# Kernel tuning notes

Measured on AMD Instinct MI355X. Metric: run time of the kernel, lower is better.

## Reference

```python
import jax, jax.numpy as jnp
import numpy as np

D_MODEL = 1024
D_STATE = 16
D_CONV = 4
EXPAND = 1
D_INNER = EXPAND * D_MODEL  # must equal D_MODEL for original dt_proj shapes to work
BATCH = 2
SEQ = 2048


def silu(x):
    return x * jax.nn.sigmoid(x)


def setup_inputs() -> dict:
    key = jax.random.key(0)
    ks = jax.random.split(key, 8)
    s = 0.02
    return {
        "x": jax.random.normal(ks[0], (BATCH, SEQ, D_MODEL), dtype=jnp.float32),
        "W_in": jax.random.normal(ks[1], (2 * D_INNER, D_MODEL), dtype=jnp.float32) * s,
        "conv_w": jax.random.normal(ks[2], (D_INNER, D_CONV), dtype=jnp.float32) * s,
        "conv_b": jnp.zeros((D_INNER,), dtype=jnp.float32),
        "W_dt": jax.random.normal(ks[3], (D_INNER, D_INNER), dtype=jnp.float32) * s,
        "b_dt": jnp.zeros((D_INNER,), dtype=jnp.float32),
        "A_log": jnp.zeros((D_INNER, D_STATE), dtype=jnp.float32),  # torch: log(ones)=0
        "Bp": jax.random.normal(ks[4], (D_INNER, D_STATE), dtype=jnp.float32),
        "Cp": jax.random.normal(ks[5], (D_INNER, D_STATE), dtype=jnp.float32),
        "Dp": jnp.ones((D_INNER,), dtype=jnp.float32),
        "W_out": jax.random.normal(ks[6], (D_MODEL, D_INNER), dtype=jnp.float32) * s,
    }


def reference(x, W_in, conv_w, conv_b, W_dt, b_dt, A_log, Bp, Cp, Dp, W_out):
    B, L, _ = x.shape
    # in_proj then split into ssm branch and gating residual
    xr = x @ W_in.T                               # (B, L, 2*D_INNER)
    x_proj, res = jnp.split(xr, 2, axis=-1)       # each (B, L, D_INNER)

    # causal depthwise conv1d (kernel D_CONV), == torch conv1d(padding=K-1)[..., :L]
    xp = jnp.pad(x_proj, ((0, 0), (D_CONV - 1, 0), (0, 0)))
    xc = conv_b + sum(conv_w[:, k] * xp[:, k:k + L, :] for k in range(D_CONV))
    xc = silu(xc)                                 # (B, L, D_INNER)

    # selective SSM scan
    delta = jax.nn.softplus(xc @ W_dt.T + b_dt)   # (B, L, D_INNER)
    A = -jnp.exp(A_log)                           # (D_INNER, D_STATE)
    dA = jnp.exp(delta[..., None] * A)            # (B, L, D_INNER, D_STATE)
    dBx = delta[..., None] * Bp * xc[..., None]   # (B, L, D_INNER, D_STATE)

    def step(h, inp):
        dA_t, dBx_t = inp                         # (B, D_INNER, D_STATE)
        h = dA_t * h + dBx_t
        y = jnp.einsum('bdn,dn->bd', h, Cp)
        return h, y

    h0 = jnp.zeros((B, D_INNER, D_STATE), dtype=x.dtype)
    _, ys = jax.lax.scan(step, h0, (dA.transpose(1, 0, 2, 3), dBx.transpose(1, 0, 2, 3)))
    x_ssm = ys.transpose(1, 0, 2) + xc * Dp       # (B, L, D_INNER)

    return (x_ssm * silu(res)) @ W_out.T          # (B, L, D_MODEL)
```

## Files before the change

kernel.cpp:

```cpp
#include <hip/hip_runtime.h>

typedef unsigned short u16;
typedef __bf16 bf16;
typedef bf16 bf16x8 __attribute__((ext_vector_type(8)));
typedef float f32x16 __attribute__((ext_vector_type(16)));

#define SEQ     2048
#define BATCH   2
#define DM      1024
#define DI      1024
#define NROW    (BATCH*SEQ)
#define NSTATE  16
#define NCHUNK  64
#define CLEN    32
#define BK      64

static_assert(SEQ == NCHUNK * CLEN, "chunking must cover SEQ");

__device__ __forceinline__ u16 f2bf(float f) {
  unsigned u = __builtin_bit_cast(unsigned, f);
  u += 0x7FFFu + ((u >> 16) & 1u);
  return (u16)(u >> 16);
}
__device__ __forceinline__ float bf2f(u16 u) {
  return __builtin_bit_cast(float, (unsigned)u << 16);
}
__device__ __forceinline__ float sigm(float x) { return 1.f / (1.f + __expf(-x)); }

__global__ __launch_bounds__(256) void k_cvt_all(
    const float* __restrict__ x, const float* __restrict__ Win,
    const float* __restrict__ Wdt, const float* __restrict__ Wout,
    u16* __restrict__ xbf, u16* __restrict__ winbf,
    u16* __restrict__ wdtbf, u16* __restrict__ woutbf)
{
  long i = (long)blockIdx.x * 256 + threadIdx.x;
  const float* src; u16* dst; long off;
  if (i < 1048576)            { src = x;    dst = xbf;    off = i; }
  else if (i < 1572864)       { src = Win;  dst = winbf;  off = i - 1048576; }
  else if (i < 1835008)       { src = Wdt;  dst = wdtbf;  off = i - 1572864; }
  else                        { src = Wout; dst = woutbf; off = i - 1835008; }
  float4 v = reinterpret_cast<const float4*>(src)[off];
  ushort4 o;
  o.x = f2bf(v.x); o.y = f2bf(v.y); o.z = f2bf(v.z); o.w = f2bf(v.w);
  reinterpret_cast<ushort4*>(dst)[off] = o;
}


__device__ __forceinline__ void gload16(const u16* g, u16* l) {
  __builtin_amdgcn_global_load_lds((const __attribute__((address_space(1))) void*)g,
                                   (__attribute__((address_space(3))) void*)l,
                                   16, 0, 0);
}

template<int EPI, int BM, int BN, int GX>
__global__ __launch_bounds__(256, 2) void k_gemm(
    const u16* __restrict__ A, const u16* __restrict__ B,
    float* __restrict__ outf, u16* __restrict__ outb, u16* __restrict__ outb2,
    const float* __restrict__ bias, int M, int N, int K)
{
  constexpr int MI_ = BM / 64;
  constexpr int NI_ = BN / 64;
  __shared__ __align__(16) u16 sA[2 * BM * BK];
  __shared__ __align__(16) u16 sB[2 * BN * BK];
  const int t = threadIdx.x;
  const int wave = t >> 6, lane = t & 63;
  const int la = lane & 31, hi = lane >> 5;
  const int wr = wave >> 1, wc = wave & 1;

  const int nwg = gridDim.x;
  const int bid = blockIdx.x;
  const int wg  = (bid & 7) * (nwg >> 3) + (bid >> 3);
  const long bm = (long)(wg / GX) * BM;
  const long bn = (long)(wg % GX) * BN;

  f32x16 acc[MI_][NI_] = {};

  const int srow = t >> 3;
  const int gslot8 = (((t & 7) ^ (srow & 7)) * 8);
  const u16* gA0 = A + (bm + srow) * (long)K + gslot8;
  const u16* gB0 = B + (bn + srow) * (long)K + gslot8;

  auto STAGE = [&](int buf, int k0) {
    #pragma unroll
    for (int i = 0; i < BM / 32; ++i)
      gload16(gA0 + (long)i * 32 * K + k0,
              &sA[buf * (BM * BK) + i * 2048 + wave * 512]);
    #pragma unroll
    for (int i = 0; i < BN / 32; ++i)
      gload16(gB0 + (long)i * 32 * K + k0,
              &sB[buf * (BN * BK) + i * 2048 + wave * 512]);
  };

  const int xr = la & 7;
  STAGE(0, 0);
  __syncthreads();
  int cur = 0;
  for (int k0 = 0; k0 < K; k0 += BK) {
    if (k0 + BK < K) STAGE(cur ^ 1, k0 + BK);
    const u16* pa = &sA[cur * (BM * BK)];
    const u16* pb = &sB[cur * (BN * BK)];
    bf16x8 af[4][MI_], bfr[4][NI_];
    #pragma unroll
    for (int ks = 0; ks < 4; ++ks) {
      const int co = ((ks * 2 + hi) ^ xr) * 8;
      #pragma unroll
      for (int mi = 0; mi < MI_; ++mi)
        af[ks][mi] = *reinterpret_cast<const bf16x8*>(
            pa + (wr * (BM / 2) + mi * 32 + la) * BK + co);
      #pragma unroll
      for (int ni = 0; ni < NI_; ++ni)
        bfr[ks][ni] = *reinterpret_cast<const bf16x8*>(
            pb + (wc * (BN / 2) + ni * 32 + la) * BK + co);
    }
    #pragma unroll
    for (int ks = 0; ks < 4; ++ks)
      #pragma unroll
      for (int mi = 0; mi < MI_; ++mi)
        #pragma unroll
        for (int ni = 0; ni < NI_; ++ni)
          acc[mi][ni] = __builtin_amdgcn_mfma_f32_32x32x16_bf16(
              af[ks][mi], bfr[ks][ni], acc[mi][ni], 0, 0, 0);
    __syncthreads();
    cur ^= 1;
  }

  #pragma unroll
  for (int mi = 0; mi < MI_; ++mi) {
    const long rowb = bm + wr * (BM / 2) + mi * 32 + 4 * hi;
    #pragma unroll
    for (int ni = 0; ni < NI_; ++ni) {
      const long col = bn + wc * (BN / 2) + ni * 32 + la;
      #pragma unroll
      for (int q = 0; q < 4; ++q)
        #pragma unroll
        for (int j = 0; j < 4; ++j) {
          const float v = acc[mi][ni][q * 4 + j];
          const long r = rowb + q * 8 + j;
          if (EPI == 0) {
            outf[r * N + col] = v;
          } else if (EPI == 1) {
            if (bn < DI) outb[r * DI + col] = f2bf(v);
            else         outb2[r * DI + (col - DI)] = f2bf(v * sigm(v));
          } else {
            float z = v + bias[col];
            outb[r * N + col] = f2bf(fmaxf(z, 0.f) + log1pf(__expf(-fabsf(z))));
          }
        }
    }
  }
}

__global__ void k_conv(const u16* __restrict__ xproj, const float* __restrict__ convw,
                       const float* __restrict__ convb, u16* __restrict__ xcbf)
{
  const int idx = blockIdx.x * 256 + threadIdx.x;
  const int d = idx & (DI - 1);
  const int m = idx >> 10;
  const int l = m & (SEQ - 1);
  float acc = convb[d];
  #pragma unroll
  for (int k = 0; k < 4; ++k) {
    int ls = l + k - 3;
    if (ls >= 0)
      acc = fmaf(convw[d * 4 + k], bf2f(xproj[(long)(m + k - 3) * DI + d]), acc);
  }
  float s = acc * sigm(acc);
  xcbf[idx] = f2bf(s);
}

__global__ __launch_bounds__(256) void k_scanA(
    const u16* __restrict__ delta, const u16* __restrict__ xc,
    const float* __restrict__ A_log, const float* __restrict__ Bp,
    float* __restrict__ hfin, float* __restrict__ sumdt_buf)
{
  const int tid = threadIdx.x, blk = blockIdx.x;
  const int d = (blk & 3) * 256 + tid;
  const int c = (blk >> 2) & (NCHUNK - 1);
  const int b = blk >> 8;
  float Aa[NSTATE], Bb[NSTATE], h[NSTATE];
  #pragma unroll
  for (int n = 0; n < NSTATE; ++n) {
    Aa[n] = -__expf(A_log[d * NSTATE + n]);
    Bb[n] = Bp[d * NSTATE + n];
    h[n] = 0.f;
  }
  const long base = ((long)(b * SEQ + c * CLEN)) * DI + d;
  float sdt = 0.f;
  for (int i = 0; i < CLEN; ++i) {
    float dt = bf2f(delta[base + (long)i * DI]);
    float x  = bf2f(xc[base + (long)i * DI]);
    sdt += dt;
    float dx = dt * x;
    #pragma unroll
    for (int n = 0; n < NSTATE; ++n) {
      float da = __expf(dt * Aa[n]);
      h[n] = fmaf(da, h[n], dx * Bb[n]);
    }
  }
  const long sb = ((long)(b * NCHUNK + c) * NSTATE) * DI + d;
  #pragma unroll
  for (int n = 0; n < NSTATE; ++n) hfin[sb + (long)n * DI] = h[n];
  sumdt_buf[(long)(b * NCHUNK + c) * DI + d] = sdt;
}

__global__ __launch_bounds__(256) void k_combine(
    const float* __restrict__ hfin, const float* __restrict__ sumdt_buf,
    const float* __restrict__ A_log, float* __restrict__ hstart)
{
  const int idx = blockIdx.x * 256 + threadIdx.x;
  const int d = idx & (DI - 1);
  const int n = (idx >> 10) & (NSTATE - 1);
  const int b = idx >> 14;
  const float Aa = -__expf(A_log[d * NSTATE + n]);
  float h = 0.f;
  for (int c = 0; c < NCHUNK; ++c) {
    const long sb = ((long)(b * NCHUNK + c) * NSTATE + n) * DI + d;
    hstart[sb] = h;
    float sdt = sumdt_buf[(long)(b * NCHUNK + c) * DI + d];
    h = fmaf(__expf(Aa * sdt), h, hfin[sb]);
  }
}

__global__ __launch_bounds__(256) void k_scanB(
    const u16* __restrict__ delta, const u16* __restrict__ xc,
    const float* __restrict__ A_log, const float* __restrict__ Bp,
    const float* __restrict__ Cp, const float* __restrict__ Dp,
    const u16* __restrict__ sres, const float* __restrict__ hstart,
    u16* __restrict__ gated)
{
  const int tid = threadIdx.x, blk = blockIdx.x;
  const int d = (blk & 3) * 256 + tid;
  const int c = (blk >> 2) & (NCHUNK - 1);
  const int b = blk >> 8;
  float Aa[NSTATE], Bb[NSTATE], Cc[NSTATE], h[NSTATE];
  #pragma unroll
  for (int n = 0; n < NSTATE; ++n) {
    Aa[n] = -__expf(A_log[d * NSTATE + n]);
    Bb[n] = Bp[d * NSTATE + n];
    Cc[n] = Cp[d * NSTATE + n];
  }
  const float Dd = Dp[d];
  const long sb = ((long)(b * NCHUNK + c) * NSTATE) * DI + d;
  #pragma unroll
  for (int n = 0; n < NSTATE; ++n) h[n] = hstart[sb + (long)n * DI];
  const long base = ((long)(b * SEQ + c * CLEN)) * DI + d;
  for (int i = 0; i < CLEN; ++i) {
    float dt = bf2f(delta[base + (long)i * DI]);
    float x  = bf2f(xc[base + (long)i * DI]);
    float dx = dt * x;
    float y = 0.f;
    #pragma unroll
    for (int n = 0; n < NSTATE; ++n) {
      float da = __expf(dt * Aa[n]);
      h[n] = fmaf(da, h[n], dx * Bb[n]);
      y = fmaf(h[n], Cc[n], y);
    }
    float xs = fmaf(x, Dd, y);
    float g = xs * bf2f(sres[base + (long)i * DI]);
    gated[base + (long)i * DI] = f2bf(g);
  }
}

extern "C" void kernel_launch(void* const* d_in, const int* in_sizes, int n_in,
                              void* d_out, int out_size, void* d_ws, size_t ws_size,
                              hipStream_t stream)
{
  const float* x      = (const float*)d_in[0];
  const float* W_in   = (const float*)d_in[1];
  const float* conv_w = (const float*)d_in[2];
  const float* conv_b = (const float*)d_in[3];
  const float* W_dt   = (const float*)d_in[4];
  const float* b_dt   = (const float*)d_in[5];
  const float* A_log  = (const float*)d_in[6];
  const float* Bp     = (const float*)d_in[7];
  const float* Cp     = (const float*)d_in[8];
  const float* Dp     = (const float*)d_in[9];
  const float* W_out  = (const float*)d_in[10];
  float* out = (float*)d_out;

  const long MD = (long)NROW * DI;

  char* ws = (char*)d_ws;
  u16*   xproj_bf = (u16*)ws;               ws += MD * 2;
  u16*   silu_bf  = (u16*)ws;               ws += MD * 2;
  u16*   delta_bf = (u16*)ws;               ws += MD * 2;
  u16*   xc_bf    = (u16*)ws;               ws += MD * 2;
  u16*   xbf      = (u16*)ws;               ws += MD * 2;
  u16*   Win_bf   = (u16*)ws;               ws += (long)2 * DI * DM * 2;
  u16*   Wdt_bf   = (u16*)ws;               ws += (long)DI * DI * 2;
  u16*   Wout_bf  = (u16*)ws;               ws += (long)DM * DI * 2;
  float* hfin     = (float*)ws;             ws += (long)BATCH * NCHUNK * NSTATE * DI * 4;
  float* sumdt    = (float*)ws;             ws += (long)BATCH * NCHUNK * DI * 4;
  float* hstart   = (float*)ws;             ws += (long)BATCH * NCHUNK * NSTATE * DI * 4;

  u16* gated = xbf;

  k_cvt_all<<<dim3(8192), dim3(256), 0, stream>>>(
      x, W_in, W_dt, W_out, xbf, Win_bf, Wdt_bf, Wout_bf);

  k_gemm<1, 128, 128, 16><<<dim3(512), dim3(256), 0, stream>>>(
      xbf, Win_bf, nullptr, xproj_bf, silu_bf, nullptr, NROW, 2 * DI, DM);

  k_conv<<<dim3((unsigned)(MD / 256)), dim3(256), 0, stream>>>(
      xproj_bf, conv_w, conv_b, xc_bf);

  k_gemm<2, 64, 64, 16><<<dim3(1024), dim3(256), 0, stream>>>(
      xc_bf, Wdt_bf, nullptr, delta_bf, nullptr, b_dt, NROW, DI, DI);

  k_scanA<<<dim3(BATCH * NCHUNK * (DI / 256)), dim3(256), 0, stream>>>(
      delta_bf, xc_bf, A_log, Bp, hfin, sumdt);
  k_combine<<<dim3(BATCH * NSTATE * DI / 256), dim3(256), 0, stream>>>(
      hfin, sumdt, A_log, hstart);
  k_scanB<<<dim3(BATCH * NCHUNK * (DI / 256)), dim3(256), 0, stream>>>(
      delta_bf, xc_bf, A_log, Bp, Cp, Dp, silu_bf, hstart, gated);

  k_gemm<0, 64, 64, 16><<<dim3(1024), dim3(256), 0, stream>>>(
      gated, Wout_bf, out, nullptr, nullptr, nullptr, NROW, DM, DI);
}
```

Baseline: 157.2 us.

## Fuse chunk-scan pass A into delta GEMM epilogue and vectorize conv

The delta GEMM epilogue now keeps the softplus outputs in shared memory and runs the first chunked-scan pass inside the same block. Each block handles two 32-step chunks over 64 channels, with two threads per channel each owning 8 states. This removes the separate k_scanA launch and its re-read of delta from global memory. The conv kernel now processes 8 channels per thread with vector loads and stores, setprio is raised around the MFMA loop, and the output GEMM gets a launch-bounds occupancy hint of 4. The trade-off is a longer, serial epilogue tail in the GEMM and higher register pressure.

```diff
diff --git a/kernel.cpp b/kernel.cpp
--- a/kernel.cpp
+++ b/kernel.cpp
@@ -52,11 +52,14 @@
                                    16, 0, 0);
 }
 
-template<int EPI, int BM, int BN, int GX>
-__global__ __launch_bounds__(256, 2) void k_gemm(
+template<int EPI, int BM, int BN, int GX, int MINW>
+__global__ __launch_bounds__(256, MINW) void k_gemm(
     const u16* __restrict__ A, const u16* __restrict__ B,
     float* __restrict__ outf, u16* __restrict__ outb, u16* __restrict__ outb2,
-    const float* __restrict__ bias, int M, int N, int K)
+    const float* __restrict__ bias,
+    const float* __restrict__ A_log, const float* __restrict__ Bp,
+    float* __restrict__ hfin, float* __restrict__ sumdt,
+    int M, int N, int K)
 {
   constexpr int MI_ = BM / 64;
   constexpr int NI_ = BN / 64;
@@ -112,6 +115,7 @@
         bfr[ks][ni] = *reinterpret_cast<const bf16x8*>(
             pb + (wc * (BN / 2) + ni * 32 + la) * BK + co);
     }
+    __builtin_amdgcn_s_setprio(1);
     #pragma unroll
     for (int ks = 0; ks < 4; ++ks)
       #pragma unroll
@@ -120,9 +124,12 @@
         for (int ni = 0; ni < NI_; ++ni)
           acc[mi][ni] = __builtin_amdgcn_mfma_f32_32x32x16_bf16(
               af[ks][mi], bfr[ks][ni], acc[mi][ni], 0, 0, 0);
+    __builtin_amdgcn_s_setprio(0);
     __syncthreads();
     cur ^= 1;
   }
+
+  float* sDelta = (float*)sA;
 
   #pragma unroll
   for (int mi = 0; mi < MI_; ++mi) {
@@ -141,66 +148,83 @@
           } else if (EPI == 1) {
             if (bn < DI) outb[r * DI + col] = f2bf(v);
             else         outb2[r * DI + (col - DI)] = f2bf(v * sigm(v));
-          } else {
+          } else if (EPI == 3) {
             float z = v + bias[col];
-            outb[r * N + col] = f2bf(fmaxf(z, 0.f) + log1pf(__expf(-fabsf(z))));
+            float sp = fmaxf(z, 0.f) + log1pf(__expf(-fabsf(z)));
+            outb[r * N + col] = f2bf(sp);
+            sDelta[(int)(r - bm) * 64 + (int)(col - bn)] = sp;
           }
         }
     }
   }
-}
-
-__global__ void k_conv(const u16* __restrict__ xproj, const float* __restrict__ convw,
-                       const float* __restrict__ convb, u16* __restrict__ xcbf)
+
+  if (EPI == 3) {
+    __syncthreads();
+    const int pair = t >> 1, half = t & 1;
+    const int clocal = pair >> 6;
+    const int dl = pair & 63;
+    const int d = (int)bn + dl;
+    const int b = (int)(bm >> 11);
+    const int cglob = (int)((bm & 2047) >> 5) + clocal;
+    const long grow0 = bm + clocal * 32;
+    float Aa[8], Bb[8], h[8];
+    #pragma unroll
+    for (int n = 0; n < 8; ++n) {
+      Aa[n] = -__expf(A_log[d * NSTATE + half * 8 + n]);
+      Bb[n] = Bp[d * NSTATE + half * 8 + n];
+      h[n] = 0.f;
+    }
+    float sdt = 0.f;
+    for (int i = 0; i < CLEN; ++i) {
+      float dt = sDelta[(clocal * 32 + i) * 64 + dl];
+      float xv = bf2f(A[(grow0 + i) * (long)K + d]);
+      sdt += dt;
+      float dx = dt * xv;
+      #pragma unroll
+      for (int n = 0; n < 8; ++n) {
+        float da = __expf(dt * Aa[n]);
+        h[n] = fmaf(da, h[n], dx * Bb[n]);
+      }
+    }
+    const long hb = ((long)(b * NCHUNK + cglob) * NSTATE + half * 8) * DI + d;
+    #pragma unroll
+    for (int n = 0; n < 8; ++n) hfin[hb + (long)n * DI] = h[n];
+    if (half == 0) sumdt[(long)(b * NCHUNK + cglob) * DI + d] = sdt;
+  }
+}
+
+__global__ __launch_bounds__(256) void k_conv(
+    const u16* __restrict__ xproj, const float* __restrict__ convw,
+    const float* __restrict__ convb, u16* __restrict__ xcbf)
 {
   const int idx = blockIdx.x * 256 + threadIdx.x;
-  const int d = idx & (DI - 1);
-  const int m = idx >> 10;
-  const int l = m & (SEQ - 1);
-  float acc = convb[d];
+  const int d0 = (idx & 127) * 8;
+  const int m  = idx >> 7;
+  const int l  = m & (SEQ - 1);
+  float acc[8];
+  #pragma unroll
+  for (int di = 0; di < 8; ++di) acc[di] = convb[d0 + di];
   #pragma unroll
   for (int k = 0; k < 4; ++k) {
-    int ls = l + k - 3;
-    if (ls >= 0)
-      acc = fmaf(convw[d * 4 + k], bf2f(xproj[(long)(m + k - 3) * DI + d]), acc);
-  }
-  float s = acc * sigm(acc);
-  xcbf[idx] = f2bf(s);
-}
-
-__global__ __launch_bounds__(256) void k_scanA(
-    const u16* __restrict__ delta, const u16* __restrict__ xc,
-    const float* __restrict__ A_log, const float* __restrict__ Bp,
-    float* __restrict__ hfin, float* __restrict__ sumdt_buf)
-{
-  const int tid = threadIdx.x, blk = blockIdx.x;
-  const int d = (blk & 3) * 256 + tid;
-  const int c = (blk >> 2) & (NCHUNK - 1);
-  const int b = blk >> 8;
-  float Aa[NSTATE], Bb[NSTATE], h[NSTATE];
-  #pragma unroll
-  for (int n = 0; n < NSTATE; ++n) {
-    Aa[n] = -__expf(A_log[d * NSTATE + n]);
-    Bb[n] = Bp[d * NSTATE + n];
-    h[n] = 0.f;
-  }
-  const long base = ((long)(b * SEQ + c * CLEN)) * DI + d;
-  float sdt = 0.f;
-  for (int i = 0; i < CLEN; ++i) {
-    float dt = bf2f(delta[base + (long)i * DI]);
-    float x  = bf2f(xc[base + (long)i * DI]);
-    sdt += dt;
-    float dx = dt * x;
-    #pragma unroll
-    for (int n = 0; n < NSTATE; ++n) {
-      float da = __expf(dt * Aa[n]);
-      h[n] = fmaf(da, h[n], dx * Bb[n]);
-    }
-  }
-  const long sb = ((long)(b * NCHUNK + c) * NSTATE) * DI + d;
-  #pragma unroll
-  for (int n = 0; n < NSTATE; ++n) hfin[sb + (long)n * DI] = h[n];
-  sumdt_buf[(long)(b * NCHUNK + c) * DI + d] = sdt;
+    if (l + k - 3 >= 0) {
+      ushort4 v2 = *reinterpret_cast<const ushort4*>(&xproj[(long)(m + k - 3) * DI + d0]);
+      ushort4 v3 = *reinterpret_cast<const ushort4*>(&xproj[(long)(m + k - 3) * DI + d0 + 4]);
+      const u16 vv[8] = {v2.x, v2.y, v2.z, v2.w, v3.x, v3.y, v3.z, v3.w};
+      #pragma unroll
+      for (int di = 0; di < 8; ++di)
+        acc[di] = fmaf(convw[(d0 + di) * 4 + k], bf2f(vv[di]), acc[di]);
+    }
+  }
+  ushort4 o0, o1;
+  u16 ov[8];
+  #pragma unroll
+  for (int di = 0; di < 8; ++di) {
+    float s = acc[di] * sigm(acc[di]);
+    ov[di] = f2bf(s);
+  }
+  o0 = {ov[0], ov[1], ov[2], ov[3]}; o1 = {ov[4], ov[5], ov[6], ov[7]};
+  *reinterpret_cast<ushort4*>(&xcbf[(long)m * DI + d0]) = o0;
+  *reinterpret_cast<ushort4*>(&xcbf[(long)m * DI + d0 + 4]) = o1;
 }
 
 __global__ __launch_bounds__(256) void k_combine(
@@ -298,22 +322,23 @@
   k_cvt_all<<<dim3(8192), dim3(256), 0, stream>>>(
       x, W_in, W_dt, W_out, xbf, Win_bf, Wdt_bf, Wout_bf);
 
-  k_gemm<1, 128, 128, 16><<<dim3(512), dim3(256), 0, stream>>>(
-      xbf, Win_bf, nullptr, xproj_bf, silu_bf, nullptr, NROW, 2 * DI, DM);
-
-  k_conv<<<dim3((unsigned)(MD / 256)), dim3(256), 0, stream>>>(
+  k_gemm<1, 128, 128, 16, 2><<<dim3(512), dim3(256), 0, stream>>>(
+      xbf, Win_bf, nullptr, xproj_bf, silu_bf, nullptr,
+      nullptr, nullptr, nullptr, nullptr, NROW, 2 * DI, DM);
+
+  k_conv<<<dim3((unsigned)(MD / 8 / 256)), dim3(256), 0, stream>>>(
       xproj_bf, conv_w, conv_b, xc_bf);
 
-  k_gemm<2, 64, 64, 16><<<dim3(1024), dim3(256), 0, stream>>>(
-      xc_bf, Wdt_bf, nullptr, delta_bf, nullptr, b_dt, NROW, DI, DI);
-
-  k_scanA<<<dim3(BATCH * NCHUNK * (DI / 256)), dim3(256), 0, stream>>>(
-      delta_bf, xc_bf, A_log, Bp, hfin, sumdt);
+  k_gemm<3, 64, 64, 16, 2><<<dim3(1024), dim3(256), 0, stream>>>(
+      xc_bf, Wdt_bf, nullptr, delta_bf, nullptr, b_dt,
+      A_log, Bp, hfin, sumdt, NROW, DI, DI);
+
   k_combine<<<dim3(BATCH * NSTATE * DI / 256), dim3(256), 0, stream>>>(
       hfin, sumdt, A_log, hstart);
   k_scanB<<<dim3(BATCH * NCHUNK * (DI / 256)), dim3(256), 0, stream>>>(
       delta_bf, xc_bf, A_log, Bp, Cp, Dp, silu_bf, hstart, gated);
 
-  k_gemm<0, 64, 64, 16><<<dim3(1024), dim3(256), 0, stream>>>(
-      gated, Wout_bf, out, nullptr, nullptr, nullptr, NROW, DM, DI);
-}
+  k_gemm<0, 64, 64, 16, 4><<<dim3(1024), dim3(256), 0, stream>>>(
+      gated, Wout_bf, out, nullptr, nullptr, nullptr,
+      nullptr, nullptr, nullptr, nullptr, NROW, DM, DI);
+}
```

Result: slower. 165.9 us (+5.5%).
